# Kernel tuning notes

Measured on AMD Instinct MI355X. Metric: run time of the kernel, lower is better.

The kernel has to match this reference:

```python
import jax, jax.numpy as jnp
import numpy as np

# ---- static config (matches init_kwargs) ----
B, S, E = 1, 2048, 2048
H, G, D = 32, 8, 64            # query heads, kv groups, head_dim
GS = H // G                    # group size = 4
SW = 128                       # sliding window
LAYER_IDX = 0                  # even -> sliding-window mask active
ROPE_BASE = 10000.0
ORIG_CTX = 4096.0              # yarn_original_context_length
YARN_SCALE = 2.0               # yarn_scaling_factor
BETA_FAST, BETA_SLOW = 32.0, 1.0


def _rope_sincos(position_ids):
    # YaRN-adjusted RoPE angles, computed directly at position_ids.
    freqs = 1.0 / ROPE_BASE ** (jnp.arange(0, D, 2, dtype=jnp.float32) / D)  # [D/2]
    wave_len = 2.0 * jnp.pi / freqs
    low = ORIG_CTX / BETA_FAST
    high = ORIG_CTX / BETA_SLOW
    t = jnp.clip((wave_len - low) / (high - low), 0.0, 1.0)
    eff = freqs * (1.0 - t) + (freqs / YARN_SCALE) * t
    conc = 0.1 * jnp.log(jnp.float32(YARN_SCALE)) + 1.0
    ang = position_ids[..., None].astype(jnp.float32) * eff * conc           # [B,S,D/2]
    ang = jnp.concatenate([ang, ang], axis=-1)                               # [B,S,D]
    # add head axis for broadcast over [B,H,S,D]
    return jnp.sin(ang)[:, None], jnp.cos(ang)[:, None]


def _apply_rope(x, sin, cos):
    x1, x2 = x[..., : D // 2], x[..., D // 2 :]
    rotated = jnp.concatenate([-x2, x1], axis=-1)
    return x * cos + rotated * sin


def setup_inputs() -> dict:
    key = jax.random.key(0)
    ks = jax.random.split(key, 6)
    x = jax.random.normal(ks[0], (B, S, E), dtype=jnp.float32)
    position_ids = jnp.broadcast_to(jnp.arange(S, dtype=jnp.int32), (B, S))
    # additive causal mask: -inf above the diagonal
    i = jnp.arange(S)[:, None]
    j = jnp.arange(S)[None, :]
    attn_mask = jnp.where(j > i, -jnp.inf, 0.0).astype(jnp.float32)[None, None]  # [1,1,S,S]
    sc = 0.02
    Wqkv = jax.random.normal(ks[1], ((H + 2 * G) * D, E), dtype=jnp.float32) * sc
    bqkv = jax.random.normal(ks[2], ((H + 2 * G) * D,), dtype=jnp.float32) * sc
    Wout = jax.random.normal(ks[3], (E, H * D), dtype=jnp.float32) * sc
    bout = jax.random.normal(ks[4], (E,), dtype=jnp.float32) * sc
    sinks = jax.random.normal(ks[5], (1, H, 1, 1), dtype=jnp.float32)
    return {"x": x, "position_ids": position_ids, "attn_mask": attn_mask,
            "Wqkv": Wqkv, "bqkv": bqkv, "Wout": Wout, "bout": bout, "sinks": sinks}


def reference(x, position_ids, attn_mask, Wqkv, bqkv, Wout, bout, sinks):
    b, s, _ = x.shape
    qkv = (x @ Wqkv.T + bqkv).reshape(b, s, H + 2 * G, D)
    Q = qkv[:, :, :H].transpose(0, 2, 1, 3)              # [B,H,S,D]
    K = qkv[:, :, H : H + G].transpose(0, 2, 1, 3)       # [B,G,S,D]
    V = qkv[:, :, H + G :].transpose(0, 2, 1, 3)         # [B,G,S,D]

    sin, cos = _rope_sincos(position_ids)
    Q = _apply_rope(Q, sin, cos)
    K = _apply_rope(K, sin, cos)

    # GQA: group query heads, no K/V duplication
    Qg = Q.reshape(b, G, GS, s, D)
    scores = jnp.einsum("bgmqd,bgkd->bgmqk", Qg, K) / (D ** 0.5)  # [B,G,GS,S,S]
    scores = scores.reshape(b, H, s, s) + attn_mask

    # sliding-window mask (layer_idx even, kv_len > sliding_window)
    if LAYER_IDX % 2 == 0 and s > SW:
        i = jnp.arange(s)[:, None]
        j = jnp.arange(s)[None, :]
        scores = jnp.where(j <= i - SW, -jnp.inf, scores)

    # learned sink logit prepended before softmax, then dropped
    sink = jnp.broadcast_to(sinks, (b, H, s, 1))
    attn = jax.nn.softmax(jnp.concatenate([sink, scores], axis=-1), axis=-1)[..., 1:]

    ctx = jnp.einsum("bgmqk,bgkd->bgmqd", attn.reshape(b, G, GS, s, s), V)
    ctx = ctx.reshape(b, H, s, D).transpose(0, 2, 1, 3).reshape(b, s, H * D)
    return ctx @ Wout.T + bout
```

## Files before the change

### kernel.cpp

```cpp
#include <hip/hip_runtime.h>
#include <cstdint>

#define S_LEN 2048
#define EMB   2048
#define NHEAD 32
#define NKV   8
#define HDIM  64
#define NQKV  3072

typedef __attribute__((ext_vector_type(8))) short bf16x8;
typedef __attribute__((ext_vector_type(4))) float f32x4;

#define GPTR const __attribute__((address_space(1))) void*
#define LPTR __attribute__((address_space(3))) void*

__device__ __forceinline__ unsigned short f2bf(float f){
  union { float f; unsigned int u; } v; v.f = f;
  unsigned int r = v.u + 0x7FFFu + ((v.u >> 16) & 1u);
  return (unsigned short)(r >> 16);
}
__device__ __forceinline__ float bf2f(unsigned short u){
  union { unsigned int u; float f; } v; v.u = ((unsigned int)u) << 16;
  return v.f;
}
__device__ __forceinline__ float yarn_eff(float ifr){
  const float freq = __expf(-ifr * (9.210340371976184f / 32.0f));
  const float wl = 6.283185307179586f / freq;
  float t = fminf(fmaxf((wl - 128.0f) * (1.0f / 3968.0f), 0.f), 1.f);
  return freq * (1.0f - 0.5f * t) * 1.0693147180559945f;
}

__global__ __launch_bounds__(256) void cvt3_kernel(const float* __restrict__ a, unsigned short* __restrict__ da, int na,
                                                   const float* __restrict__ b, unsigned short* __restrict__ db, int nb,
                                                   const float* __restrict__ c, unsigned short* __restrict__ dc, int nc){
  int i = blockIdx.x * 256 + threadIdx.x;
  const float* s; unsigned short* d;
  if (i < na){ s = a; d = da; }
  else if (i < na + nb){ s = b; d = db; i -= na; }
  else if (i < na + nb + nc){ s = c; d = dc; i -= na + nb; }
  else return;
  const float4 v = ((const float4*)s)[i];
  ushort4 o;
  o.x = f2bf(v.x); o.y = f2bf(v.y); o.z = f2bf(v.z); o.w = f2bf(v.w);
  ((ushort4*)d)[i] = o;
}


template<int OUT_BF16, int ROPE, int TM>
__global__ __launch_bounds__(256) void gemm_bt(const unsigned short* __restrict__ A,
                                               const unsigned short* __restrict__ B,
                                               const float* __restrict__ bias,
                                               void* __restrict__ Cout,
                                               const int* __restrict__ pos,
                                               int M, int N, int K){
  constexpr int MI = TM / 32;
  constexpr int AI = TM / 64;
  __shared__ unsigned short As[4*TM*32];
  __shared__ unsigned short Bs[4*128*32];
  const int tid  = threadIdx.x;
  const int lane = tid & 63;
  const int wid  = tid >> 6;
  const int m0 = blockIdx.y * TM;
  const int n0 = blockIdx.x * 128;
  const int wm = (wid >> 1) * (TM/2);
  const int wn = (wid & 1) * 64;
  const int fm = lane & 15;
  const int quad = lane >> 4;
  const int csw8 = (quad ^ ((fm >> 1) & 3)) * 8;

  f32x4 acc[MI][4];
#pragma unroll
  for (int i = 0; i < MI; ++i)
#pragma unroll
    for (int j = 0; j < 4; ++j) acc[i][j] = {0.f, 0.f, 0.f, 0.f};

  const int srow = lane >> 2;
  const int scol = (((lane & 3) ^ ((lane >> 3) & 3)) * 8);
  const unsigned short* Ag = A + (size_t)(m0 + wid*(TM/4) + srow) * K + scol;
  const unsigned short* Bg = B + (size_t)(n0 + wid*32 + srow) * K + scol;
  unsigned short* AsW = &As[(wid*(TM/4))*32];
  unsigned short* BsW = &Bs[(wid*32)*32];

  auto stage_sub = [&](int k0, int slot){
    unsigned short* dA = AsW + slot*(TM*32);
    unsigned short* dB = BsW + slot*(128*32);
#pragma unroll
    for (int t = 0; t < AI; ++t)
      __builtin_amdgcn_global_load_lds((GPTR)(Ag + k0 + (size_t)(t*16)*K), (LPTR)(dA + t*16*32), 16, 0, 0);
    __builtin_amdgcn_global_load_lds((GPTR)(Bg + k0), (LPTR)dB, 16, 0, 0);
    __builtin_amdgcn_global_load_lds((GPTR)(Bg + k0 + (size_t)16*K), (LPTR)(dB + 16*32), 16, 0, 0);
  };

  stage_sub(0, 0);  stage_sub(32, 1);
  stage_sub(64, 2); stage_sub(96, 3);

  const int KEP = K >> 6;
  for (int e = 0; e < KEP; ++e){
    const int buf = e & 1;
    if (e + 1 < KEP){
      if constexpr (TM == 128) asm volatile("s_waitcnt vmcnt(8)" ::: "memory");
      else                     asm volatile("s_waitcnt vmcnt(6)" ::: "memory");
    } else {
      asm volatile("s_waitcnt vmcnt(0)" ::: "memory");
    }
    asm volatile("s_barrier" ::: "memory");

    bf16x8 af[2][MI], bfr[2][4];
#pragma unroll
    for (int s = 0; s < 2; ++s){
      const unsigned short* Ab = As + (buf*2+s)*(TM*32);
      const unsigned short* Bb = Bs + (buf*2+s)*(128*32);
#pragma unroll
      for (int i = 0; i < MI; ++i) af[s][i]  = *(const bf16x8*)&Ab[(wm + i*16 + fm)*32 + csw8];
#pragma unroll
      for (int j = 0; j < 4; ++j)  bfr[s][j] = *(const bf16x8*)&Bb[(wn + j*16 + fm)*32 + csw8];
    }
#pragma unroll
    for (int s = 0; s < 2; ++s)
#pragma unroll
      for (int i = 0; i < MI; ++i)
#pragma unroll
        for (int j = 0; j < 4; ++j)
          acc[i][j] = __builtin_amdgcn_mfma_f32_16x16x32_bf16(af[s][i], bfr[s][j], acc[i][j], 0, 0, 0);

    asm volatile("s_barrier" ::: "memory");
    if (e + 2 < KEP){
      stage_sub((e+2)*64,      buf*2);
      stage_sub((e+2)*64 + 32, buf*2 + 1);
    }
  }

  float bv[4];
#pragma unroll
  for (int j = 0; j < 4; ++j) bv[j] = bias[n0 + wn + j*16 + fm];

  const bool dorope = ROPE && (n0 + wn) < 2560;
  if (dorope){
    const float eff0 = yarn_eff((float)fm);
    const float eff1 = yarn_eff((float)(fm + 16));
#pragma unroll
    for (int i = 0; i < MI; ++i){
#pragma unroll
      for (int r = 0; r < 4; ++r){
        const int row = m0 + wm + i*16 + quad*4 + r;
        const float pp = (float)pos[row];
        float s0, c0, s1, c1;
        __sincosf(pp * eff0, &s0, &c0);
        __sincosf(pp * eff1, &s1, &c1);
        const float v0 = acc[i][0][r] + bv[0];
        const float v1 = acc[i][1][r] + bv[1];
        const float v2 = acc[i][2][r] + bv[2];
        const float v3 = acc[i][3][r] + bv[3];
        const float o0 = v0*c0 - v2*s0;
        const float o1 = v1*c1 - v3*s1;
        const float o2 = v2*c0 + v0*s0;
        const float o3 = v3*c1 + v1*s1;
        const size_t base = (size_t)row*N + n0 + wn + fm;
        if (OUT_BF16){
          unsigned short* C16 = (unsigned short*)Cout;
          C16[base +  0] = f2bf(o0); C16[base + 16] = f2bf(o1);
          C16[base + 32] = f2bf(o2); C16[base + 48] = f2bf(o3);
        } else {
          float* C32 = (float*)Cout;
          C32[base +  0] = o0; C32[base + 16] = o1;
          C32[base + 32] = o2; C32[base + 48] = o3;
        }
      }
    }
  } else {
#pragma unroll
    for (int i = 0; i < MI; ++i){
#pragma unroll
      for (int r = 0; r < 4; ++r){
        const int row = m0 + wm + i*16 + quad*4 + r;
        const size_t base = (size_t)row*N + n0 + wn + fm;
#pragma unroll
        for (int j = 0; j < 4; ++j){
          const float v = acc[i][j][r] + bv[j];
          if (OUT_BF16) ((unsigned short*)Cout)[base + j*16] = f2bf(v);
          else          ((float*)Cout)[base + j*16] = v;
        }
      }
    }
  }
}

__global__ __launch_bounds__(384) void gemm_qkv(const unsigned short* __restrict__ A,
                                                const unsigned short* __restrict__ B,
                                                const float* __restrict__ bias,
                                                unsigned short* __restrict__ C,
                                                const int* __restrict__ pos){
  constexpr int N = 3072, K = 2048;
  __shared__ unsigned short Lds[2*20480];
  const int tid  = threadIdx.x;
  const int lane = tid & 63;
  const int wid  = tid >> 6;
  const int m0 = blockIdx.y * 128;
  const int n0 = blockIdx.x * 192;
  const int wm = (wid & 1) * 64;
  const int wn = (wid >> 1) * 64;
  const int fm = lane & 15;
  const int quad = lane >> 4;
  const int csw8 = (quad ^ ((fm >> 1) & 3)) * 8;

  f32x4 acc[4][4];
#pragma unroll
  for (int i = 0; i < 4; ++i)
#pragma unroll
    for (int j = 0; j < 4; ++j) acc[i][j] = {0.f, 0.f, 0.f, 0.f};

  const int srow = lane >> 2;
  const int scol = (((lane & 3) ^ ((lane >> 3) & 3)) * 8);

  const unsigned short* gsrc[7];
  int ldst[7];
#pragma unroll
  for (int i = 0; i < 7; ++i){
    const int u  = wid + i*6;
    const int uu = (u < 40) ? u : 0;
    const int sub = uu / 20;
    const int v   = uu % 20;
    const int isA = (v < 8) ? 1 : 0;
    const int rc  = isA ? v : (v - 8);
    const unsigned short* gp = isA ? (A + (size_t)(m0 + rc*16 + srow) * K)
                                   : (B + (size_t)(n0 + rc*16 + srow) * K);
    gsrc[i] = gp + scol + sub*32;
    ldst[i] = isA ? (sub*4096 + rc*512) : (8192 + sub*6144 + rc*512);
  }

  auto stage = [&](int t, int poff){
    const size_t koff = (size_t)t * 64;
#pragma unroll
    for (int i = 0; i < 6; ++i)
      __builtin_amdgcn_global_load_lds((GPTR)(gsrc[i] + koff), (LPTR)(Lds + ldst[i] + poff), 16, 0, 0);
    if (wid < 4)
      __builtin_amdgcn_global_load_lds((GPTR)(gsrc[6] + koff), (LPTR)(Lds + ldst[6] + poff), 16, 0, 0);
  };

  stage(0, 0);
  stage(1, 20480);

  constexpr int KEP = K >> 6;
  for (int e = 0; e < KEP; ++e){
    const int poff = (e & 1) * 20480;
    if (e + 1 < KEP){
      if (wid < 4) asm volatile("s_waitcnt vmcnt(7)" ::: "memory");
      else         asm volatile("s_waitcnt vmcnt(6)" ::: "memory");
    } else {
      asm volatile("s_waitcnt vmcnt(0)" ::: "memory");
    }
    asm volatile("s_barrier" ::: "memory");

    bf16x8 af[2][4], bfr[2][4];
#pragma unroll
    for (int s = 0; s < 2; ++s){
      const unsigned short* Ab = Lds + poff + s*4096;
      const unsigned short* Bb = Lds + poff + 8192 + s*6144;
#pragma unroll
      for (int i = 0; i < 4; ++i) af[s][i]  = *(const bf16x8*)&Ab[(wm + i*16 + fm)*32 + csw8];
#pragma unroll
      for (int j = 0; j < 4; ++j) bfr[s][j] = *(const bf16x8*)&Bb[(wn + j*16 + fm)*32 + csw8];
    }
#pragma unroll
    for (int s = 0; s < 2; ++s)
#pragma unroll
      for (int i = 0; i < 4; ++i)
#pragma unroll
        for (int j = 0; j < 4; ++j)
          acc[i][j] = __builtin_amdgcn_mfma_f32_16x16x32_bf16(af[s][i], bfr[s][j], acc[i][j], 0, 0, 0);

    asm volatile("s_barrier" ::: "memory");
    if (e + 2 < KEP) stage(e+2, poff);
  }

  float bv[4];
#pragma unroll
  for (int j = 0; j < 4; ++j) bv[j] = bias[n0 + wn + j*16 + fm];

  const bool dorope = (n0 + wn) < 2560;
  if (dorope){
    const float eff0 = yarn_eff((float)fm);
    const float eff1 = yarn_eff((float)(fm + 16));
#pragma unroll
    for (int i = 0; i < 4; ++i){
#pragma unroll
      for (int r = 0; r < 4; ++r){
        const int row = m0 + wm + i*16 + quad*4 + r;
        const float pp = (float)pos[row];
        float s0, c0, s1, c1;
        __sincosf(pp * eff0, &s0, &c0);
        __sincosf(pp * eff1, &s1, &c1);
        const float v0 = acc[i][0][r] + bv[0];
        const float v1 = acc[i][1][r] + bv[1];
        const float v2 = acc[i][2][r] + bv[2];
        const float v3 = acc[i][3][r] + bv[3];
        const float o0 = v0*c0 - v2*s0;
        const float o1 = v1*c1 - v3*s1;
        const float o2 = v2*c0 + v0*s0;
        const float o3 = v3*c1 + v1*s1;
        const size_t base = (size_t)row*N + n0 + wn + fm;
        C[base +  0] = f2bf(o0); C[base + 16] = f2bf(o1);
        C[base + 32] = f2bf(o2); C[base + 48] = f2bf(o3);
      }
    }
  } else {
#pragma unroll
    for (int i = 0; i < 4; ++i){
#pragma unroll
      for (int r = 0; r < 4; ++r){
        const int row = m0 + wm + i*16 + quad*4 + r;
        const size_t base = (size_t)row*N + n0 + wn + fm;
#pragma unroll
        for (int j = 0; j < 4; ++j)
          C[base + j*16] = f2bf(acc[i][j][r] + bv[j]);
      }
    }
  }
}

__global__ __launch_bounds__(256) void attn_kernel(const unsigned short* __restrict__ qkv,
                                                   const float* __restrict__ sinks,
                                                   unsigned short* __restrict__ ctxb,
                                                   const float* __restrict__ wout,
                                                   unsigned short* __restrict__ wob){
  const int h  = blockIdx.y;
  const int q0 = blockIdx.x * 64;
  const int g  = h >> 2;
  const int tid  = threadIdx.x;
  const int lane = tid & 63;
  const int wid  = tid >> 6;
  const int fm   = lane & 15;
  const int quad = lane >> 4;

  __shared__ unsigned short Ks[2*64*40];
  __shared__ unsigned short Vt[2*64*34];
  __shared__ unsigned short Pl[4*2*16*40];

  const int qrow = q0 + wid*16 + fm;
  bf16x8 aq[2];
#pragma unroll
  for (int ks = 0; ks < 2; ++ks)
    aq[ks] = *(const bf16x8*)(qkv + (size_t)qrow*NQKV + h*HDIM + ks*32 + quad*8);

  f32x4 o[4];
#pragma unroll
  for (int nt = 0; nt < 4; ++nt) o[nt] = {0.f, 0.f, 0.f, 0.f};
  float m_[4], l_[4];
#pragma unroll
  for (int r = 0; r < 4; ++r){ m_[r] = -30000.f; l_[r] = 0.f; }

  const int qbase = q0 + wid*16 + quad*4;
  int cs0 = q0 - 128; if (cs0 < 0) cs0 = 0;
  unsigned short* plw = &Pl[wid*1280];

  for (int cs = cs0; cs <= q0; cs += 64){
    __syncthreads();
#pragma unroll
    for (int it = 0; it < 2; ++it){
      const int e = (tid + it*256) * 8;
      const int key = e >> 6, d0 = e & 63;
      const unsigned short* kp = qkv + (size_t)(cs + key)*NQKV + EMB + g*HDIM + d0;
      *(bf16x8*)&Ks[(d0>>5)*2560 + key*40 + (d0 & 31)] = *(const bf16x8*)kp;
      const bf16x8 vv = *(const bf16x8*)(kp + NKV*HDIM);
      const unsigned short* vs = (const unsigned short*)&vv;
      unsigned short* vt = &Vt[(key>>5)*2176 + (key & 31)];
#pragma unroll
      for (int j = 0; j < 8; ++j) vt[(d0 + j)*34] = vs[j];
    }
    __syncthreads();

    f32x4 sa[4];
#pragma unroll
    for (int nt = 0; nt < 4; ++nt){
      sa[nt] = {0.f, 0.f, 0.f, 0.f};
#pragma unroll
      for (int ks = 0; ks < 2; ++ks){
        const bf16x8 bk = *(const bf16x8*)&Ks[ks*2560 + (nt*16 + fm)*40 + quad*8];
        sa[nt] = __builtin_amdgcn_mfma_f32_16x16x32_bf16(aq[ks], bk, sa[nt], 0, 0, 0);
      }
    }

#pragma unroll
    for (int nt = 0; nt < 4; ++nt){
      const int key = cs + nt*16 + fm;
#pragma unroll
      for (int r = 0; r < 4; ++r){
        const float s = sa[nt][r] * 0.125f;
        const bool ok = (unsigned)(qbase + r - key) < 128u;
        sa[nt][r] = ok ? s : -1e30f;
      }
    }

#pragma unroll
    for (int r = 0; r < 4; ++r){
      float t = fmaxf(fmaxf(sa[0][r], sa[1][r]), fmaxf(sa[2][r], sa[3][r]));
#pragma unroll
      for (int off = 1; off < 16; off <<= 1) t = fmaxf(t, __shfl_xor(t, off, 64));
      const float nm = fmaxf(m_[r], t);
      const float al = __expf(m_[r] - nm);
#pragma unroll
      for (int nt = 0; nt < 4; ++nt) sa[nt][r] = __expf(sa[nt][r] - nm);
      float ts = (sa[0][r] + sa[1][r]) + (sa[2][r] + sa[3][r]);
#pragma unroll
      for (int off = 1; off < 16; off <<= 1) ts += __shfl_xor(ts, off, 64);
      l_[r] = l_[r]*al + ts;
      m_[r] = nm;
#pragma unroll
      for (int nt = 0; nt < 4; ++nt) o[nt][r] *= al;
    }

#pragma unroll
    for (int nt = 0; nt < 4; ++nt)
#pragma unroll
      for (int r = 0; r < 4; ++r)
        plw[(nt>>1)*640 + (quad*4 + r)*40 + (nt&1)*16 + fm] = f2bf(sa[nt][r]);
    __asm__ volatile("s_waitcnt lgkmcnt(0)" ::: "memory");

    bf16x8 pa[2];
#pragma unroll
    for (int ks = 0; ks < 2; ++ks)
      pa[ks] = *(const bf16x8*)&plw[ks*640 + fm*40 + quad*8];
    const unsigned int* vb = (const unsigned int*)Vt;
#pragma unroll
    for (int nt = 0; nt < 4; ++nt){
#pragma unroll
      for (int ks = 0; ks < 2; ++ks){
        const int ui = ks*1088 + (nt*16 + fm)*17 + quad*4;
        union { unsigned int u[4]; bf16x8 v; } bb;
        bb.u[0] = vb[ui+0]; bb.u[1] = vb[ui+1]; bb.u[2] = vb[ui+2]; bb.u[3] = vb[ui+3];
        o[nt] = __builtin_amdgcn_mfma_f32_16x16x32_bf16(pa[ks], bb.v, o[nt], 0, 0, 0);
      }
    }
  }

  const float snk = sinks[h];
#pragma unroll
  for (int r = 0; r < 4; ++r){
    const float nm = fmaxf(m_[r], snk);
    const float e  = __expf(m_[r] - nm);
    const float denom = l_[r]*e + __expf(snk - nm);
    const float sc = e / denom;
    const size_t row = (size_t)(qbase + r)*EMB + h*HDIM;
#pragma unroll
    for (int nt = 0; nt < 4; ++nt)
      ctxb[row + nt*16 + fm] = f2bf(o[nt][r] * sc);
  }

  const int gtid = (blockIdx.y * 32 + blockIdx.x) * 256 + tid;
#pragma unroll
  for (int it = 0; it < 4; ++it){
    const int i4 = gtid + it * (32*32*256);
    const float4 v = ((const float4*)wout)[i4];
    ushort4 ow;
    ow.x = f2bf(v.x); ow.y = f2bf(v.y); ow.z = f2bf(v.z); ow.w = f2bf(v.w);
    ((ushort4*)wob)[i4] = ow;
  }
}

extern "C" void kernel_launch(void* const* d_in, const int* in_sizes, int n_in,
                              void* d_out, int out_size, void* d_ws, size_t ws_size,
                              hipStream_t stream){
  const float* x     = (const float*)d_in[0];
  const int*   pos   = (const int*)  d_in[1];
  const float* Wqkv  = (const float*)d_in[3];
  const float* bqkv  = (const float*)d_in[4];
  const float* Wout  = (const float*)d_in[5];
  const float* bout  = (const float*)d_in[6];
  const float* sinks = (const float*)d_in[7];

  char* ws = (char*)d_ws;
  unsigned short* xb   = (unsigned short*)(ws);
  unsigned short* wqb  = (unsigned short*)(ws + 8388608);
  unsigned short* wob  = (unsigned short*)(ws + 20971520);
  unsigned short* qkv  = (unsigned short*)(ws + 29360128);
  unsigned short* ctxb = (unsigned short*)(ws + 41943040);

  cvt3_kernel<<<dim3(10240), dim3(256), 0, stream>>>(x, xb, 1048576,
                                                     Wqkv, wqb, 1572864,
                                                     nullptr, nullptr, 0);

  gemm_qkv<<<dim3(16, 16), dim3(384), 0, stream>>>(xb, wqb, bqkv, qkv, pos);
  attn_kernel<<<dim3(32, 32), dim3(256), 0, stream>>>(qkv, sinks, ctxb, Wout, wob);
  gemm_bt<0,0,64><<<dim3(16, 32), dim3(256), 0, stream>>>(ctxb, wob, bout, d_out, nullptr, 2048, 2048, 2048);
}
```

Before: 198.4 us.

## Triple-buffer QKV GEMM LDS stages with one barrier per k-step

The QKV projection GEMM moves from two to three LDS buffers. The load for stage e+2 is now issued before computing stage e, which removes the second barrier per iteration and gives global-to-LDS copies more time to overlap with MFMA work. MFMA bursts are also wrapped in s_setprio, and fragment loads are interleaved per k-substep. This raises LDS use to about 120 KB per block, which may reduce occupancy, and the vmcnt accounting must stay correct for the new ordering. The (i&1)/(i>>1) row remapping is applied consistently to the fragment loads and the epilogue, so it leaves the output unchanged.

```diff
diff --git a/kernel.cpp b/kernel.cpp
--- a/kernel.cpp
+++ b/kernel.cpp
@@ -191,7 +191,8 @@
                                                 unsigned short* __restrict__ C,
                                                 const int* __restrict__ pos){
   constexpr int N = 3072, K = 2048;
-  __shared__ unsigned short Lds[2*20480];
+  constexpr int PS = 20480;
+  __shared__ unsigned short Lds[3*PS];
   const int tid  = threadIdx.x;
   const int lane = tid & 63;
   const int wid  = tid >> 6;
@@ -216,61 +217,64 @@
   int ldst[7];
 #pragma unroll
   for (int i = 0; i < 7; ++i){
-    const int u  = wid + i*6;
-    const int uu = (u < 40) ? u : 0;
-    const int sub = uu / 20;
-    const int v   = uu % 20;
+    int u = wid + i*6;
+    if (u >= 40) u = 0;
+    const int sub = (u >= 20) ? 1 : 0;
+    const int v   = u - sub*20;
     const int isA = (v < 8) ? 1 : 0;
-    const int rc  = isA ? v : (v - 8);
-    const unsigned short* gp = isA ? (A + (size_t)(m0 + rc*16 + srow) * K)
-                                   : (B + (size_t)(n0 + rc*16 + srow) * K);
+    const unsigned short* gp = isA ? (A + (size_t)(m0 + v*16 + srow) * K)
+                                   : (B + (size_t)(n0 + (v-8)*16 + srow) * K);
     gsrc[i] = gp + scol + sub*32;
-    ldst[i] = isA ? (sub*4096 + rc*512) : (8192 + sub*6144 + rc*512);
-  }
-
-  auto stage = [&](int t, int poff){
+    ldst[i] = isA ? (sub*4096 + v*512) : (8192 + sub*6144 + (v-8)*512);
+  }
+
+  auto stage = [&](int t, int boff){
     const size_t koff = (size_t)t * 64;
 #pragma unroll
     for (int i = 0; i < 6; ++i)
-      __builtin_amdgcn_global_load_lds((GPTR)(gsrc[i] + koff), (LPTR)(Lds + ldst[i] + poff), 16, 0, 0);
+      __builtin_amdgcn_global_load_lds((GPTR)(gsrc[i] + koff), (LPTR)(Lds + ldst[i] + boff), 16, 0, 0);
     if (wid < 4)
-      __builtin_amdgcn_global_load_lds((GPTR)(gsrc[6] + koff), (LPTR)(Lds + ldst[6] + poff), 16, 0, 0);
+      __builtin_amdgcn_global_load_lds((GPTR)(gsrc[6] + koff), (LPTR)(Lds + ldst[6] + boff), 16, 0, 0);
   };
 
   stage(0, 0);
-  stage(1, 20480);
+  stage(1, PS);
+  if (wid < 4) asm volatile("s_waitcnt vmcnt(7)" ::: "memory");
+  else         asm volatile("s_waitcnt vmcnt(6)" ::: "memory");
+  asm volatile("s_barrier" ::: "memory");
 
   constexpr int KEP = K >> 6;
   for (int e = 0; e < KEP; ++e){
-    const int poff = (e & 1) * 20480;
+    const int boff = (e % 3) * PS;
+    if (e + 2 < KEP) stage(e + 2, ((e + 2) % 3) * PS);
+
+#pragma unroll
+    for (int s = 0; s < 2; ++s){
+      const unsigned short* Ab = Lds + boff + s*4096;
+      const unsigned short* Bb = Lds + boff + 8192 + s*6144;
+      bf16x8 af[4], bf[4];
+#pragma unroll
+      for (int i = 0; i < 4; ++i) af[i] = *(const bf16x8*)&Ab[(wm + ((i&1)*16) + ((i>>1)*32) + fm)*32 + csw8];
+#pragma unroll
+      for (int j = 0; j < 4; ++j) bf[j] = *(const bf16x8*)&Bb[(wn + j*16 + fm)*32 + csw8];
+      __builtin_amdgcn_s_setprio(1);
+#pragma unroll
+      for (int i = 0; i < 4; ++i)
+#pragma unroll
+        for (int j = 0; j < 4; ++j)
+          acc[i][j] = __builtin_amdgcn_mfma_f32_16x16x32_bf16(af[i], bf[j], acc[i][j], 0, 0, 0);
+      __builtin_amdgcn_s_setprio(0);
+    }
+
     if (e + 1 < KEP){
-      if (wid < 4) asm volatile("s_waitcnt vmcnt(7)" ::: "memory");
-      else         asm volatile("s_waitcnt vmcnt(6)" ::: "memory");
-    } else {
-      asm volatile("s_waitcnt vmcnt(0)" ::: "memory");
-    }
-    asm volatile("s_barrier" ::: "memory");
-
-    bf16x8 af[2][4], bfr[2][4];
-#pragma unroll
-    for (int s = 0; s < 2; ++s){
-      const unsigned short* Ab = Lds + poff + s*4096;
-      const unsigned short* Bb = Lds + poff + 8192 + s*6144;
-#pragma unroll
-      for (int i = 0; i < 4; ++i) af[s][i]  = *(const bf16x8*)&Ab[(wm + i*16 + fm)*32 + csw8];
-#pragma unroll
-      for (int j = 0; j < 4; ++j) bfr[s][j] = *(const bf16x8*)&Bb[(wn + j*16 + fm)*32 + csw8];
-    }
-#pragma unroll
-    for (int s = 0; s < 2; ++s)
-#pragma unroll
-      for (int i = 0; i < 4; ++i)
-#pragma unroll
-        for (int j = 0; j < 4; ++j)
-          acc[i][j] = __builtin_amdgcn_mfma_f32_16x16x32_bf16(af[s][i], bfr[s][j], acc[i][j], 0, 0, 0);
-
-    asm volatile("s_barrier" ::: "memory");
-    if (e + 2 < KEP) stage(e+2, poff);
+      if (e + 2 < KEP){
+        if (wid < 4) asm volatile("s_waitcnt vmcnt(7)" ::: "memory");
+        else         asm volatile("s_waitcnt vmcnt(6)" ::: "memory");
+      } else {
+        asm volatile("s_waitcnt vmcnt(0)" ::: "memory");
+      }
+      asm volatile("s_barrier" ::: "memory");
+    }
   }
 
   float bv[4];
@@ -285,7 +289,7 @@
     for (int i = 0; i < 4; ++i){
 #pragma unroll
       for (int r = 0; r < 4; ++r){
-        const int row = m0 + wm + i*16 + quad*4 + r;
+        const int row = m0 + wm + (i&1)*16 + (i>>1)*32 + quad*4 + r;
         const float pp = (float)pos[row];
         float s0, c0, s1, c1;
         __sincosf(pp * eff0, &s0, &c0);
@@ -308,7 +312,7 @@
     for (int i = 0; i < 4; ++i){
 #pragma unroll
       for (int r = 0; r < 4; ++r){
-        const int row = m0 + wm + i*16 + quad*4 + r;
+        const int row = m0 + wm + (i&1)*16 + (i>>1)*32 + quad*4 + r;
         const size_t base = (size_t)row*N + n0 + wn + fm;
 #pragma unroll
         for (int j = 0; j < 4; ++j)
```

New measurement: 194.5 us. 1.02x faster.
